# Optimization experiments

Hardware: AMD Instinct MI355X
Metric: run time of the kernel (lower is better)

## Reference

```python
import jax, jax.numpy as jnp
import numpy as np

HQ, HKV, D = 16, 2, 128   # num_heads_q, num_heads_kv, head_dim
G = HQ // HKV             # q heads per kv head (repeat_interleave factor)


def setup_inputs() -> dict:
    key = jax.random.key(0)
    ks = jax.random.split(key, 6)
    B, T, C = 2, 2048, 2048
    def w(k, shape):
        return jax.random.normal(k, shape, jnp.float32) * (1.0 / np.sqrt(shape[0]).astype(np.float32))
    x = jax.random.normal(ks[0], (B, T, C), jnp.float32)
    Wq = w(ks[1], (C, HQ * D))
    Wk = w(ks[2], (C, HKV * D))
    Wv = w(ks[3], (C, HKV * D))
    Wo = w(ks[4], (HQ * D, C))
    Wg = w(ks[5], (C, HQ))
    # causal mask: True where attention is disallowed (j > i)
    mask = jnp.triu(jnp.ones((T, T), dtype=bool), k=1)[None, None]  # (1,1,T,T)
    return {"x": x, "mask": mask, "Wq": Wq, "Wk": Wk, "Wv": Wv, "Wo": Wo, "Wg": Wg}


def reference(x, mask, Wq, Wk, Wv, Wo, Wg):
    B, T, C = x.shape
    # repeat_interleave(G, dim=heads) means q head h uses kv head h // G,
    # so group q heads as (HKV, G) instead of materializing repeated K/V.
    q = (x @ Wq).reshape(B, T, HKV, G, D).transpose(0, 2, 3, 1, 4)  # (B,HKV,G,T,D)
    k = (x @ Wk).reshape(B, T, HKV, D).transpose(0, 2, 1, 3)        # (B,HKV,T,D)
    v = (x @ Wv).reshape(B, T, HKV, D).transpose(0, 2, 1, 3)        # (B,HKV,T,D)
    scale = jnp.float32(1.0 / np.sqrt(D))
    scores = jnp.einsum('bkgtd,bksd->bkgts', q, k) * scale          # (B,HKV,G,T,T)
    scores = jnp.where(mask[:, None], jnp.float32(-1e9), scores)    # causal fill
    attn = jax.nn.softmax(scores, axis=-1)
    # post-softmax sigmoid gate, one scalar per (batch, q-head, query token)
    gates = jax.nn.sigmoid(x @ Wg)                                   # (B,T,HQ)
    gates = gates.transpose(0, 2, 1).reshape(B, HKV, G, T)           # (B,HKV,G,T)
    out = jnp.einsum('bkgts,bksd->btkgd', attn * gates[..., None], v)
    out = out.reshape(B, T, HQ * D)
    return out @ Wo
```

## Files before the change

kernel.cpp:

```cpp
#include <hip/hip_runtime.h>
#include <hip/hip_bf16.h>
#include <math.h>

#define HQ 16
#define HKV 2
#define D 128
#define B_SZ 2
#define T_SZ 2048
#define C_SZ 2048
#define QKVN 2688

#define C_Q 0.12753102f
#define C_G 1.44269504f

typedef __attribute__((ext_vector_type(8))) short short8;
typedef __attribute__((ext_vector_type(4))) float floatx4;

static __device__ __forceinline__ float fexp2(float x) {
    return __builtin_amdgcn_exp2f(x);
}

static __device__ __forceinline__ unsigned short f2b(float f) {
    union { float f; unsigned u; } x; x.f = f;
    return (unsigned short)((x.u + 0x7fffu + ((x.u >> 16) & 1u)) >> 16);
}

static __device__ __forceinline__ unsigned int pk2(float a, float b) {
    float2 t; t.x = a; t.y = b;
    __hip_bfloat162 h = __float22bfloat162_rn(t);
    return *(unsigned int*)&h;
}

static __device__ __forceinline__ void load_lds16(const void* g, void* l) {
    __builtin_amdgcn_global_load_lds(
        (const __attribute__((address_space(1))) void*)g,
        (__attribute__((address_space(3))) void*)l,
        16, 0, 0);
}

static __device__ __forceinline__ void tr32(
    const float* __restrict__ in, unsigned short* __restrict__ out,
    int R, int Cc, float premul, int bx, int by, float (*t)[33])
{
    const int bc = bx * 32, br = by * 32;
    const int tid = threadIdx.x;
    const int r = tid >> 3, c4 = (tid & 7) * 4;
    float4 v = *(const float4*)(in + (size_t)(br + r) * Cc + bc + c4);
    t[r][c4 + 0] = v.x; t[r][c4 + 1] = v.y; t[r][c4 + 2] = v.z; t[r][c4 + 3] = v.w;
    __syncthreads();
    ushort4 o;
    o.x = f2b(t[c4 + 0][r] * premul); o.y = f2b(t[c4 + 1][r] * premul);
    o.z = f2b(t[c4 + 2][r] * premul); o.w = f2b(t[c4 + 3][r] * premul);
    *(ushort4*)(out + (size_t)(bc + r) * R + br + c4) = o;
}

__global__ __launch_bounds__(256) void prep_kernel(
    const float* __restrict__ x,  const float* __restrict__ Wq,
    const float* __restrict__ Wk, const float* __restrict__ Wv,
    const float* __restrict__ Wo, const float* __restrict__ Wg,
    unsigned short* __restrict__ xb, unsigned short* __restrict__ Wqkvt,
    unsigned short* __restrict__ Wot)
{
    __shared__ float t[32][33];
    const int bid = blockIdx.x;
    const int tid = threadIdx.x;
    if (bid < 4096) {
        int i = bid * 2048 + tid * 8;
        float4 a = *(const float4*)(x + i);
        float4 b = *(const float4*)(x + i + 4);
        ushort4 o0, o1;
        o0.x = f2b(a.x); o0.y = f2b(a.y); o0.z = f2b(a.z); o0.w = f2b(a.w);
        o1.x = f2b(b.x); o1.y = f2b(b.y); o1.z = f2b(b.z); o1.w = f2b(b.w);
        *(ushort4*)(xb + i) = o0;
        *(ushort4*)(xb + i + 4) = o1;
    } else if (bid < 8192) {
        int n = bid - 4096;
        tr32(Wq, Wqkvt, C_SZ, HQ * D, C_Q, n & 63, n >> 6, t);
    } else if (bid < 8704) {
        int n = bid - 8192;
        tr32(Wk, Wqkvt + (size_t)(HQ * D) * C_SZ, C_SZ, HKV * D, 1.0f, n & 7, n >> 3, t);
    } else if (bid < 9216) {
        int n = bid - 8704;
        tr32(Wv, Wqkvt + (size_t)(HQ * D + HKV * D) * C_SZ, C_SZ, HKV * D, 1.0f, n & 7, n >> 3, t);
    } else if (bid < 13312) {
        int n = bid - 9216;
        tr32(Wo, Wot, HQ * D, C_SZ, 1.0f, n & 63, n >> 6, t);
    } else {
        int k = (bid - 13312) * 256 + tid;
        const float4* wr = (const float4*)(Wg + (size_t)k * 16);
        float4 w0 = wr[0], w1 = wr[1], w2 = wr[2], w3 = wr[3];
        float w[16] = {w0.x, w0.y, w0.z, w0.w, w1.x, w1.y, w1.z, w1.w,
                       w2.x, w2.y, w2.z, w2.w, w3.x, w3.y, w3.z, w3.w};
        unsigned short* out = Wqkvt + (size_t)(HQ * D + 2 * HKV * D) * C_SZ;
        #pragma unroll
        for (int h = 0; h < 16; ++h)
            out[(size_t)h * C_SZ + k] = f2b(w[h] * C_G);
    }
}

template<int BM>
__global__ __launch_bounds__(512, 2) void gemm256(
    const unsigned short* __restrict__ A, const unsigned short* __restrict__ Bt,
    float* __restrict__ Cf, unsigned short* __restrict__ Cb,
    int Nreal, int K, int out_bf16)
{
    constexpr int MT = BM / 32;
    constexpr int LA = BM / 64;
    constexpr int VM = LA + 4;
    __shared__ __align__(16) unsigned short SM[2][(BM + 256) * 64];

    const int tid = threadIdx.x;
    const int lane = tid & 63, wave = tid >> 6;
    const int l15 = lane & 15, quad = lane >> 4;
    const int wm = wave >> 2, wn = wave & 3;
    const int bm0 = blockIdx.y * BM, bn0 = blockIdx.x * 256;
    const int NT = K >> 6;

    unsigned aoff[LA], boff[4];
    #pragma unroll
    for (int j = 0; j < LA; ++j) {
        int c = j * 512 + tid, r = c >> 3, sb = c & 7;
        aoff[j] = (unsigned)(((bm0 + r) * K + ((sb ^ (r & 7)) << 3)) * 2);
    }
    #pragma unroll
    for (int j = 0; j < 4; ++j) {
        int c = j * 512 + tid, r = c >> 3, sb = c & 7;
        boff[j] = (unsigned)(((bn0 + r) * K + ((sb ^ (r & 7)) << 3)) * 2);
    }

    floatx4 zero = {0.f, 0.f, 0.f, 0.f};
    floatx4 acc[MT][4];
    #pragma unroll
    for (int i = 0; i < MT; ++i)
        #pragma unroll
        for (int j = 0; j < 4; ++j) acc[i][j] = zero;

    auto STAGE = [&](int b, int t) {
        #pragma unroll
        for (int j = 0; j < LA; ++j)
            load_lds16((const char*)A + aoff[j] + (size_t)t * 128,
                       &SM[b][(j * 512 + wave * 64) * 8]);
        #pragma unroll
        for (int j = 0; j < 4; ++j)
            load_lds16((const char*)Bt + boff[j] + (size_t)t * 128,
                       &SM[b][BM * 64 + (j * 512 + wave * 64) * 8]);
    };

    auto RD = [&](short8 (&FA)[MT], short8 (&FB)[4], int b, int kk) {
        const unsigned short* Sa = &SM[b][0];
        const unsigned short* Sb = &SM[b][BM * 64];
        const int swz = ((kk << 2) + quad) ^ (l15 & 7);
        #pragma unroll
        for (int mt = 0; mt < MT; ++mt)
            FA[mt] = *(const short8*)&Sa[(wm * (BM / 2) + mt * 16 + l15) * 64 + swz * 8];
        #pragma unroll
        for (int nt = 0; nt < 4; ++nt)
            FB[nt] = *(const short8*)&Sb[(wn * 64 + nt * 16 + l15) * 64 + swz * 8];
    };

    auto MM = [&](short8 (&FA)[MT], short8 (&FB)[4]) {
        __builtin_amdgcn_s_setprio(1);
        #pragma unroll
        for (int mt = 0; mt < MT; ++mt)
            #pragma unroll
            for (int nt = 0; nt < 4; ++nt)
                acc[mt][nt] = __builtin_amdgcn_mfma_f32_16x16x32_bf16(
                    FA[mt], FB[nt], acc[mt][nt], 0, 0, 0);
        __builtin_amdgcn_s_setprio(0);
    };

    short8 RaA[MT], RaB[4], RbA[MT], RbB[4];

    STAGE(0, 0);
    STAGE(1, 1);
    asm volatile("s_waitcnt vmcnt(%0)" :: "n"(VM) : "memory");
    __builtin_amdgcn_sched_barrier(0);
    __builtin_amdgcn_s_barrier();
    __builtin_amdgcn_sched_barrier(0);
    RD(RaA, RaB, 0, 0);

    #pragma unroll 2
    for (int t = 0; t < NT; ++t) {
        const int b = t & 1;
        RD(RbA, RbB, b, 1);
        MM(RaA, RaB);
        asm volatile("s_waitcnt lgkmcnt(0)" ::: "memory");
        __builtin_amdgcn_sched_barrier(0);
        __builtin_amdgcn_s_barrier();
        __builtin_amdgcn_sched_barrier(0);
        if (t + 2 < NT) {
            STAGE(b, t + 2);
            asm volatile("s_waitcnt vmcnt(%0)" :: "n"(VM) : "memory");
        } else if (t + 1 < NT) {
            asm volatile("s_waitcnt vmcnt(0)" ::: "memory");
        }
        __builtin_amdgcn_sched_barrier(0);
        __builtin_amdgcn_s_barrier();
        __builtin_amdgcn_sched_barrier(0);
        if (t + 1 < NT) RD(RaA, RaB, b ^ 1, 0);
        MM(RbA, RbB);
    }

    #pragma unroll
    for (int mt = 0; mt < MT; ++mt)
        #pragma unroll
        for (int nt = 0; nt < 4; ++nt) {
            const int n = bn0 + wn * 64 + nt * 16 + l15;
            if (n < Nreal) {
                #pragma unroll
                for (int r = 0; r < 4; ++r) {
                    const int m = bm0 + wm * (BM / 2) + mt * 16 + quad * 4 + r;
                    if (out_bf16) Cb[(size_t)m * Nreal + n] = f2b(acc[mt][nt][r]);
                    else          Cf[(size_t)m * Nreal + n] = acc[mt][nt][r];
                }
            }
        }
}

__global__ __launch_bounds__(256) void vtrans(
    const unsigned short* __restrict__ QKV, unsigned short* __restrict__ Vt)
{
    __shared__ unsigned short T[64][72];
    const int tid = threadIdx.x;
    const int tok0 = blockIdx.x * 64, vd0 = blockIdx.y * 64;
    const int r = tid >> 2, c = (tid & 3) * 16;
    const unsigned short* src = QKV + (size_t)(tok0 + r) * QKVN
                                    + (HQ * D + HKV * D) + vd0 + c;
    short8 v0 = *(const short8*)src;
    short8 v1 = *(const short8*)(src + 8);
    #pragma unroll
    for (int j = 0; j < 8; ++j) { T[c + j][r] = v0[j]; T[c + 8 + j][r] = v1[j]; }
    __syncthreads();
    const int b = tok0 >> 11, tl = tok0 & 2047;
    unsigned short* dst = Vt + ((size_t)b * (HKV * D) + vd0 + r) * T_SZ + tl + c;
    *(short8*)dst       = *(const short8*)&T[r][c];
    *(short8*)(dst + 8) = *(const short8*)&T[r][c + 8];
}

__global__ __launch_bounds__(256) void attn_mfma(
    const unsigned short* __restrict__ QKV, const unsigned short* __restrict__ Vt,
    unsigned short* __restrict__ Ob)
{
    __shared__ __align__(16) unsigned short SMEM[64 * 128 + 128 * 64 + 4 * 16 * 72];
    unsigned short* Ks = SMEM;
    unsigned short* Vs = SMEM + 64 * 128;
    unsigned short* Ps = SMEM + 64 * 128 + 128 * 64;
    unsigned short* Lo = SMEM;

    const int bh = blockIdx.x;
    const int qt = (int)gridDim.y - 1 - (int)blockIdx.y;
    const int b = bh >> 4, h = bh & 15, kvh = h >> 3;
    const int tid = threadIdx.x;
    const int lane = tid & 63, w = tid >> 6;
    const int l15 = lane & 15, quad = lane >> 4;
    const int q_local = w * 16 + l15;
    const float BIAS = 32.0f;

    short8 aq[4];
    {
        const unsigned short* qp = QKV + (size_t)(b * T_SZ + qt * 64 + q_local) * QKVN
                                       + h * D + quad * 8;
        #pragma unroll
        for (int kd = 0; kd < 4; ++kd) aq[kd] = *(const short8*)(qp + kd * 32);
    }

    const unsigned short* kg[4];
    const unsigned short* vg[4];
    #pragma unroll
    for (int it = 0; it < 4; ++it) {
        int Bi = it * 256 + tid;
        int kr = Bi >> 4, kc = ((Bi & 15) ^ (kr & 15)) * 8;
        kg[it] = QKV + (size_t)(b * T_SZ + kr) * QKVN + HQ * D + kvh * D + kc;
        int vr = Bi >> 3, vc = ((Bi & 7) ^ (vr & 7)) * 8;
        vg[it] = Vt + (size_t)((b * HKV + kvh) * D + vr) * T_SZ + vc;
    }

    floatx4 zero = {0.f, 0.f, 0.f, 0.f};
    floatx4 oacc[8];
    #pragma unroll
    for (int dt = 0; dt < 8; ++dt) oacc[dt] = zero;
    float l_part = 0.f;

    for (int kt = 0; kt <= qt; ++kt) {
        __syncthreads();
        #pragma unroll
        for (int it = 0; it < 4; ++it) {
            load_lds16(kg[it] + (size_t)kt * 64 * QKVN, &Ks[(it * 256 + w * 64) * 8]);
            load_lds16(vg[it] + kt * 64,                &Vs[(it * 256 + w * 64) * 8]);
        }
        __syncthreads();

        floatx4 sacc[4];
        #pragma unroll
        for (int nt = 0; nt < 4; ++nt) sacc[nt] = zero;
        #pragma unroll
        for (int kd = 0; kd < 4; ++kd)
            #pragma unroll
            for (int nt = 0; nt < 4; ++nt) {
                short8 ak = *(const short8*)&Ks[((nt * 16 + l15) * 16 + ((kd * 4 + quad) ^ l15)) * 8];
                sacc[nt] = __builtin_amdgcn_mfma_f32_16x16x32_bf16(ak, aq[kd], sacc[nt], 0, 0, 0);
            }

        float p[4][4];
        if (kt == qt) {
            #pragma unroll
            for (int nt = 0; nt < 4; ++nt)
                #pragma unroll
                for (int r = 0; r < 4; ++r) {
                    float e = fexp2(sacc[nt][r] - BIAS);
                    p[nt][r] = (nt * 16 + quad * 4 + r > q_local) ? 0.f : e;
                }
        } else {
            #pragma unroll
            for (int nt = 0; nt < 4; ++nt)
                #pragma unroll
                for (int r = 0; r < 4; ++r)
                    p[nt][r] = fexp2(sacc[nt][r] - BIAS);
        }
        #pragma unroll
        for (int nt = 0; nt < 4; ++nt) {
            l_part += (p[nt][0] + p[nt][1]) + (p[nt][2] + p[nt][3]);
            uint2 pw;
            pw.x = pk2(p[nt][0], p[nt][1]);
            pw.y = pk2(p[nt][2], p[nt][3]);
            *(uint2*)&Ps[(w * 16 + l15) * 72 + nt * 16 + quad * 4] = pw;
        }

        #pragma unroll
        for (int kk = 0; kk < 2; ++kk) {
            short8 bp = *(const short8*)&Ps[(w * 16 + l15) * 72 + kk * 32 + quad * 8];
            #pragma unroll
            for (int dt = 0; dt < 8; ++dt) {
                short8 av = *(const short8*)&Vs[((dt * 16 + l15) * 8 + ((kk * 4 + quad) ^ (l15 & 7))) * 8];
                oacc[dt] = __builtin_amdgcn_mfma_f32_16x16x32_bf16(av, bp, oacc[dt], 0, 0, 0);
            }
        }
    }

    float l = l_part;
    l += __shfl_xor(l, 16);
    l += __shfl_xor(l, 32);

    __syncthreads();
    {
        int token = b * T_SZ + qt * 64 + q_local;
        unsigned short gl = QKV[(size_t)token * QKVN + HQ * D + HKV * D * 2 + h];
        union { unsigned u; float f; } gx; gx.u = ((unsigned)gl) << 16;
        float g = 1.0f / (1.0f + fexp2(-gx.f));
        float f = g / l;
        #pragma unroll
        for (int dt = 0; dt < 8; ++dt) {
            uint2 ov;
            ov.x = pk2(oacc[dt][0] * f, oacc[dt][1] * f);
            ov.y = pk2(oacc[dt][2] * f, oacc[dt][3] * f);
            *(uint2*)&Lo[(size_t)q_local * 136 + dt * 16 + quad * 4] = ov;
        }
    }
    __syncthreads();
    {
        int row = tid >> 2, c0 = (tid & 3) * 32;
        size_t tok = (size_t)(b * T_SZ + qt * 64 + row);
        unsigned short* op = Ob + tok * (HQ * D) + h * D + c0;
        const unsigned short* lp = &Lo[(size_t)row * 136 + c0];
        short8 v0 = *(const short8*)(lp + 0);
        short8 v1 = *(const short8*)(lp + 8);
        short8 v2 = *(const short8*)(lp + 16);
        short8 v3 = *(const short8*)(lp + 24);
        *(short8*)(op + 0)  = v0; *(short8*)(op + 8)  = v1;
        *(short8*)(op + 16) = v2; *(short8*)(op + 24) = v3;
    }
}

extern "C" void kernel_launch(void* const* d_in, const int* in_sizes, int n_in,
                              void* d_out, int out_size, void* d_ws, size_t ws_size,
                              hipStream_t stream) {
    const float* x  = (const float*)d_in[0];
    const float* Wq = (const float*)d_in[2];
    const float* Wk = (const float*)d_in[3];
    const float* Wv = (const float*)d_in[4];
    const float* Wo = (const float*)d_in[5];
    const float* Wg = (const float*)d_in[6];
    float* out = (float*)d_out;

    const size_t KB = 1ull << 10;
    char* p = (char*)d_ws;
    unsigned short* xb    = (unsigned short*)(p);
    unsigned short* Ob    = xb;
    unsigned short* Wqkvt = (unsigned short*)(p + 16384 * KB);
    unsigned short* Wot   = (unsigned short*)(p + 27136 * KB);
    unsigned short* QKV   = (unsigned short*)(p + 35328 * KB);
    unsigned short* Vt    = (unsigned short*)(p + 56832 * KB);
    const int BT = B_SZ * T_SZ;

    prep_kernel<<<dim3(13320), 256, 0, stream>>>(x, Wq, Wk, Wv, Wo, Wg, xb, Wqkvt, Wot);

    gemm256<256><<<dim3(11, BT / 256), 512, 0, stream>>>(
        xb, Wqkvt, nullptr, QKV, QKVN, C_SZ, 1);

    vtrans<<<dim3(BT / 64, (HKV * D) / 64), 256, 0, stream>>>(QKV, Vt);

    attn_mfma<<<dim3(B_SZ * HQ, T_SZ / 64), 256, 0, stream>>>(QKV, Vt, Ob);

    gemm256<128><<<dim3(C_SZ / 256, BT / 128), 512, 0, stream>>>(
        Ob, Wot, out, nullptr, C_SZ, HQ * D, 0);
}
```

Measured before the change: 287.2 us.

## Fuse V transpose into QKV GEMM epilogue and register-prefetch K/V in attention

The QKV GEMM blocks that cover the V columns (bn0 == 2304) now write their tile transposed through shared memory straight into the Vt buffer, so the separate vtrans kernel and its launch go away. In the attention kernel, the direct global-to-LDS loads are replaced by register prefetch of the next K/V tile, which is stored to LDS after an explicit barrier. This is meant to overlap global loads with compute, and the kernel now declares a 3-block occupancy hint. The risks are higher register pressure in attention and a serialized four-pass transpose epilogue in the GEMM blocks that handle V.

```diff
diff --git a/kernel.cpp b/kernel.cpp
--- a/kernel.cpp
+++ b/kernel.cpp
@@ -102,7 +102,7 @@
 __global__ __launch_bounds__(512, 2) void gemm256(
     const unsigned short* __restrict__ A, const unsigned short* __restrict__ Bt,
     float* __restrict__ Cf, unsigned short* __restrict__ Cb,
-    int Nreal, int K, int out_bf16)
+    unsigned short* __restrict__ Vt, int Nreal, int K, int out_bf16)
 {
     constexpr int MT = BM / 32;
     constexpr int LA = BM / 64;
@@ -199,6 +199,38 @@
         __builtin_amdgcn_sched_barrier(0);
         if (t + 1 < NT) RD(RaA, RaB, b ^ 1, 0);
         MM(RbA, RbB);
+    }
+
+    if (Vt != nullptr && bn0 == 2304) {
+        unsigned short (*Ct)[264] = (unsigned short(*)[264])SM;
+        const int bb = bm0 >> 11;
+        const int tl = bm0 & 2047;
+        #pragma unroll
+        for (int v = 0; v < 4; ++v) {
+            __syncthreads();
+            if (wn == v) {
+                #pragma unroll
+                for (int mt = 0; mt < MT; ++mt)
+                    #pragma unroll
+                    for (int nt = 0; nt < 4; ++nt)
+                        #pragma unroll
+                        for (int r = 0; r < 4; ++r)
+                            Ct[nt * 16 + l15][wm * (BM / 2) + mt * 16 + quad * 4 + r] =
+                                f2b(acc[mt][nt][r]);
+            }
+            __syncthreads();
+            int row = tid >> 3, c0 = (tid & 7) * 32;
+            unsigned short* dst = Vt + ((size_t)bb * (HKV * D) + v * 64 + row) * T_SZ
+                                     + tl + c0;
+            const unsigned short* src = &Ct[row][c0];
+            short8 s0 = *(const short8*)(src + 0);
+            short8 s1 = *(const short8*)(src + 8);
+            short8 s2 = *(const short8*)(src + 16);
+            short8 s3 = *(const short8*)(src + 24);
+            *(short8*)(dst + 0)  = s0; *(short8*)(dst + 8)  = s1;
+            *(short8*)(dst + 16) = s2; *(short8*)(dst + 24) = s3;
+        }
+        return;
     }
 
     #pragma unroll
@@ -217,27 +249,7 @@
         }
 }
 
-__global__ __launch_bounds__(256) void vtrans(
-    const unsigned short* __restrict__ QKV, unsigned short* __restrict__ Vt)
-{
-    __shared__ unsigned short T[64][72];
-    const int tid = threadIdx.x;
-    const int tok0 = blockIdx.x * 64, vd0 = blockIdx.y * 64;
-    const int r = tid >> 2, c = (tid & 3) * 16;
-    const unsigned short* src = QKV + (size_t)(tok0 + r) * QKVN
-                                    + (HQ * D + HKV * D) + vd0 + c;
-    short8 v0 = *(const short8*)src;
-    short8 v1 = *(const short8*)(src + 8);
-    #pragma unroll
-    for (int j = 0; j < 8; ++j) { T[c + j][r] = v0[j]; T[c + 8 + j][r] = v1[j]; }
-    __syncthreads();
-    const int b = tok0 >> 11, tl = tok0 & 2047;
-    unsigned short* dst = Vt + ((size_t)b * (HKV * D) + vd0 + r) * T_SZ + tl + c;
-    *(short8*)dst       = *(const short8*)&T[r][c];
-    *(short8*)(dst + 8) = *(const short8*)&T[r][c + 8];
-}
-
-__global__ __launch_bounds__(256) void attn_mfma(
+__global__ __launch_bounds__(256, 3) void attn_mfma(
     const unsigned short* __restrict__ QKV, const unsigned short* __restrict__ Vt,
     unsigned short* __restrict__ Ob)
 {
@@ -281,14 +293,34 @@
     for (int dt = 0; dt < 8; ++dt) oacc[dt] = zero;
     float l_part = 0.f;
 
+    short8 krg[4], vrg[4];
+    #pragma unroll
+    for (int it = 0; it < 4; ++it) {
+        krg[it] = *(const short8*)(kg[it]);
+        vrg[it] = *(const short8*)(vg[it]);
+    }
+
     for (int kt = 0; kt <= qt; ++kt) {
-        __syncthreads();
+        asm volatile("s_waitcnt vmcnt(0)" ::: "memory");
+        __builtin_amdgcn_sched_barrier(0);
+        __builtin_amdgcn_s_barrier();
+        __builtin_amdgcn_sched_barrier(0);
         #pragma unroll
         for (int it = 0; it < 4; ++it) {
-            load_lds16(kg[it] + (size_t)kt * 64 * QKVN, &Ks[(it * 256 + w * 64) * 8]);
-            load_lds16(vg[it] + kt * 64,                &Vs[(it * 256 + w * 64) * 8]);
-        }
-        __syncthreads();
+            *(short8*)&Ks[(it * 256 + tid) * 8] = krg[it];
+            *(short8*)&Vs[(it * 256 + tid) * 8] = vrg[it];
+        }
+        if (kt < qt) {
+            #pragma unroll
+            for (int it = 0; it < 4; ++it) {
+                krg[it] = *(const short8*)(kg[it] + (size_t)(kt + 1) * 64 * QKVN);
+                vrg[it] = *(const short8*)(vg[it] + (kt + 1) * 64);
+            }
+        }
+        asm volatile("s_waitcnt lgkmcnt(0)" ::: "memory");
+        __builtin_amdgcn_sched_barrier(0);
+        __builtin_amdgcn_s_barrier();
+        __builtin_amdgcn_sched_barrier(0);
 
         floatx4 sacc[4];
         #pragma unroll
@@ -395,12 +427,10 @@
     prep_kernel<<<dim3(13320), 256, 0, stream>>>(x, Wq, Wk, Wv, Wo, Wg, xb, Wqkvt, Wot);
 
     gemm256<256><<<dim3(11, BT / 256), 512, 0, stream>>>(
-        xb, Wqkvt, nullptr, QKV, QKVN, C_SZ, 1);
-
-    vtrans<<<dim3(BT / 64, (HKV * D) / 64), 256, 0, stream>>>(QKV, Vt);
+        xb, Wqkvt, nullptr, QKV, Vt, QKVN, C_SZ, 1);
 
     attn_mfma<<<dim3(B_SZ * HQ, T_SZ / 64), 256, 0, stream>>>(QKV, Vt, Ob);
 
     gemm256<128><<<dim3(C_SZ / 256, BT / 128), 512, 0, stream>>>(
-        Ob, Wot, out, nullptr, C_SZ, HQ * D, 0);
-}
+        Ob, Wot, out, nullptr, nullptr, C_SZ, HQ * D, 0);
+}
```

New measurement: 289.8 us. No clear change (+0.9%).
